# Kernel optimization log

Measured on AMD Instinct MI355X. Metric: run time of the kernel, lower is better.

The kernel has to match this reference:

```python
import jax, jax.numpy as jnp
import numpy as np
import math

B, L, C_IN, D, H, FACTOR = 32, 512, 32, 512, 8, 1
E = D // H
TOP_K = int(FACTOR * math.log(L))  # 6


def setup_inputs() -> dict:
    key = jax.random.key(0)
    ks = jax.random.split(key, 14)
    s = 0.02
    f = lambda k, shp: jax.random.normal(k, shp, jnp.float32) * s
    return {
        "x": jax.random.normal(ks[0], (B, L, C_IN), jnp.float32),
        "conv_w": f(ks[1], (D, C_IN)),  # Conv1d kernel_size=1 == pointwise linear
        "conv_b": f(ks[2], (D,)),
        "wq": f(ks[3], (D, D)), "bq": f(ks[4], (D,)),
        "wk": f(ks[5], (D, D)), "bk": f(ks[6], (D,)),
        "wv": f(ks[7], (D, D)), "bv": f(ks[8], (D,)),
        "wo": f(ks[9], (D, D)), "bo": f(ks[10], (D,)),
        "lin_w": f(ks[11], (1, D)), "lin_b": f(ks[12], (1,)),
    }


def _autocorrelation(q, k, v):
    # q, k, v: [B, L, H, E]; Autoformer AutoCorrelation (inference delay agg)
    qf = jnp.fft.rfft(q.transpose(0, 2, 3, 1), axis=-1)        # [B,H,E,Lf]
    kf = jnp.fft.rfft(k.transpose(0, 2, 3, 1), axis=-1)
    corr = jnp.fft.irfft(qf * jnp.conj(kf), n=L, axis=-1)       # [B,H,E,L]
    vals = v.transpose(0, 2, 3, 1)                              # [B,H,E,L]
    mean_corr = corr.mean(axis=(1, 2))                          # [B,L]
    weights, delay = jax.lax.top_k(mean_corr, TOP_K)            # [B,k]
    w = jax.nn.softmax(weights, axis=-1)                        # [B,k]
    # gather values at (t + delay) mod L  (== doubled-values trick in torch)
    idx = (jnp.arange(L)[None, None, :] + delay[:, :, None]) % L  # [B,k,L]
    patterns = jnp.take_along_axis(
        vals[:, :, :, None, :], idx[:, None, None, :, :], axis=-1)  # [B,H,E,k,L]
    agg = jnp.einsum('bhekl,bk->bhel', patterns, w)             # [B,H,E,L]
    return agg.transpose(0, 3, 1, 2)                            # [B,L,H,E]


def reference(x, conv_w, conv_b, wq, bq, wk, bk, wv, bv, wo, bo, lin_w, lin_b):
    # pointwise conv1d projection: [B,L,C_IN] -> [B,L,D]
    h = x @ conv_w.T + conv_b
    q = (h @ wq.T + bq).reshape(B, L, H, E)
    k = (h @ wk.T + bk).reshape(B, L, H, E)
    v = (h @ wv.T + bv).reshape(B, L, H, E)
    attn_out = _autocorrelation(q, k, v).reshape(B, L, D)
    new_x = attn_out @ wo.T + bo
    out = h + new_x          # residual
    last = out[:, -1:, :]    # x[:, -1:]
    y = last @ lin_w.T + lin_b  # [B,1,1]
    return y
```

## Files before the change

kernel.cpp:

```cpp
#include <hip/hip_runtime.h>
#include <hip/hip_bf16.h>

#define LL 512
#define BB 32
#define DD 512
#define CINN 32
#define TOPK 6
#define BL (BB * LL)

typedef __attribute__((ext_vector_type(8))) short bf16x8;
typedef __attribute__((ext_vector_type(4))) float f32x4;

__device__ inline float bf2f(ushort u) {
    union { uint i; float f; } c; c.i = ((uint)u) << 16; return c.f;
}
__device__ inline ushort f2bf(float f) {
    union { float f; uint i; } c; c.f = f;
    uint i = c.i;
    return (ushort)((i + 0x7FFFu + ((i >> 16) & 1u)) >> 16);
}
__device__ inline void split_bf(float v, ushort& hi, ushort& lo) {
    hi = f2bf(v);
    lo = f2bf(v - bf2f(hi));
}

__device__ inline void gload16(const ushort* g, ushort* l) {
    __builtin_amdgcn_global_load_lds(
        (const __attribute__((address_space(1))) unsigned int*)(const void*)g,
        (__attribute__((address_space(3))) unsigned int*)(void*)l,
        16, 0, 0);
}

__device__ inline void stage_tile32(ushort* buf,
                                    const ushort* A_h, const ushort* A_l,
                                    const ushort* B_h, const ushort* B_l,
                                    int wid, int lane) {
    const int l4 = lane >> 2, sl = lane & 3;
    const ushort* src = (wid == 0) ? A_h : (wid == 1) ? A_l : (wid == 2) ? B_h : B_l;
    ushort* dst = buf + wid * 4096;
    #pragma unroll
    for (int o = 0; o < 8; ++o) {
        const int row = o * 16 + l4;
        gload16(src + (long)row * 32 + ((sl ^ ((row >> 1) & 3)) << 3),
                dst + o * 512);
    }
}

__device__ inline bf16x8 frag_ld(const ushort* sm, int r, int s) {
    return *(const bf16x8*)(sm + r * 32 + ((s ^ ((r >> 1) & 3)) << 3));
}

__device__ inline void mfma_step(const ushort* sAh, const ushort* sAl,
                                 const ushort* sBh, const ushort* sBl,
                                 f32x4 acc[4][4], int wr, int wc, int fr, int fs) {
    bf16x8 bh[4], blo[4];
    #pragma unroll
    for (int ni = 0; ni < 4; ++ni) {
        bh[ni]  = frag_ld(sBh, wc + ni * 16 + fr, fs);
        blo[ni] = frag_ld(sBl, wc + ni * 16 + fr, fs);
    }
    #pragma unroll
    for (int mi = 0; mi < 4; ++mi) {
        const bf16x8 ah = frag_ld(sAh, wr + mi * 16 + fr, fs);
        const bf16x8 al = frag_ld(sAl, wr + mi * 16 + fr, fs);
        #pragma unroll
        for (int ni = 0; ni < 4; ++ni) {
            acc[mi][ni] = __builtin_amdgcn_mfma_f32_16x16x32_bf16(ah, bh[ni],  acc[mi][ni], 0, 0, 0);
            acc[mi][ni] = __builtin_amdgcn_mfma_f32_16x16x32_bf16(ah, blo[ni], acc[mi][ni], 0, 0, 0);
            acc[mi][ni] = __builtin_amdgcn_mfma_f32_16x16x32_bf16(al, bh[ni],  acc[mi][ni], 0, 0, 0);
        }
    }
}

__global__ __launch_bounds__(256) void prep_m(
    const float* __restrict__ wq, const float* __restrict__ wk,
    const float* __restrict__ cw,
    const float* __restrict__ lin_w, const float* __restrict__ wo,
    float* __restrict__ Mpart, float* __restrict__ upart)
{
    const int tid = threadIdx.x;
    if (blockIdx.x < 64) {
        __shared__ float cws[512][32];
        __shared__ float wqsT[512][9];
        __shared__ float wksT[512][9];
        __shared__ float aqs[8][32];
        __shared__ float aks[8][32];
        for (int i = tid; i < 4096; i += 256) {
            const int d = i >> 3, q = i & 7;
            *(float4*)&cws[d][q * 4] = *(const float4*)(cw + (long)d * 32 + q * 4);
        }
        const int e0 = blockIdx.x * 8;
        for (int i = tid; i < 4096; i += 256) {
            const int e = i >> 9, d = i & 511;
            wqsT[d][e] = wq[(long)(e0 + e) * 512 + d];
            wksT[d][e] = wk[(long)(e0 + e) * 512 + d];
        }
        __syncthreads();
        const int e_loc = tid >> 5, c = tid & 31;
        float aq = 0.f, ak = 0.f;
        #pragma unroll 4
        for (int d = 0; d < 512; ++d) {
            const float cv = cws[d][c];
            aq += wqsT[d][e_loc] * cv;
            ak += wksT[d][e_loc] * cv;
        }
        aqs[e_loc][c] = aq;
        aks[e_loc][c] = ak;
        __syncthreads();
        const int c_ = tid >> 3, cq = tid & 7;
        float m0 = 0.f, m1 = 0.f, m2 = 0.f, m3 = 0.f;
        #pragma unroll
        for (int e = 0; e < 8; ++e) {
            const float a = aqs[e][c_];
            const float4 k4 = *(const float4*)&aks[e][cq * 4];
            m0 += a * k4.x; m1 += a * k4.y; m2 += a * k4.z; m3 += a * k4.w;
        }
        *(float4*)(Mpart + (long)blockIdx.x * 1024 + c_ * 32 + cq * 4) =
            make_float4(m0, m1, m2, m3);
    } else {
        const int j = blockIdx.x - 64;
        const int n0 = j * 64;
        float u0 = 0.f, u1 = 0.f;
        for (int n = 0; n < 64; ++n) {
            const float lw = lin_w[n0 + n];
            u0 += lw * wo[(long)(n0 + n) * 512 + tid];
            u1 += lw * wo[(long)(n0 + n) * 512 + tid + 256];
        }
        upart[j * 512 + tid] = u0;
        upart[j * 512 + tid + 256] = u1;
    }
}

__global__ __launch_bounds__(256) void prep_xu(
    const float* __restrict__ x,
    const float* __restrict__ Mpart, const float* __restrict__ upart,
    const float* __restrict__ wv,
    ushort* __restrict__ Xh, ushort* __restrict__ Xl,
    ushort* __restrict__ Uh, ushort* __restrict__ Ul,
    float* __restrict__ v2part)
{
    const int tid = threadIdx.x;
    if (blockIdx.x < 64) {
        __shared__ float Ml[32][36];
        float s0 = 0.f, s1 = 0.f, s2 = 0.f, s3 = 0.f;
        for (int p = 0; p < 64; ++p) {
            const float4 v = *(const float4*)(Mpart + (long)p * 1024 + tid * 4);
            s0 += v.x; s1 += v.y; s2 += v.z; s3 += v.w;
        }
        const int mc_ = tid >> 3, mq = tid & 7;
        *(float4*)&Ml[mc_][mq * 4] = make_float4(s0, s1, s2, s3);
        __syncthreads();

        const long row = (long)blockIdx.x * 256 + tid;
        float xr[32], ur[32];
        #pragma unroll
        for (int q = 0; q < 8; ++q)
            *(float4*)&xr[q * 4] = *(const float4*)(x + row * 32 + q * 4);
        #pragma unroll
        for (int c2 = 0; c2 < 32; ++c2) {
            float s = 0.f;
            #pragma unroll
            for (int q = 0; q < 8; ++q) {
                const float4 m = *(const float4*)&Ml[c2][q * 4];
                s += m.x * xr[q * 4] + m.y * xr[q * 4 + 1]
                   + m.z * xr[q * 4 + 2] + m.w * xr[q * 4 + 3];
            }
            ur[c2] = s;
        }
        #pragma unroll
        for (int q = 0; q < 8; ++q) {
            ushort xh4[4], xl4[4], uh4[4], ul4[4];
            #pragma unroll
            for (int j = 0; j < 4; ++j) {
                split_bf(xr[q * 4 + j], xh4[j], xl4[j]);
                split_bf(ur[q * 4 + j], uh4[j], ul4[j]);
            }
            *(ushort4*)(Xh + row * 32 + q * 4) = make_ushort4(xh4[0], xh4[1], xh4[2], xh4[3]);
            *(ushort4*)(Xl + row * 32 + q * 4) = make_ushort4(xl4[0], xl4[1], xl4[2], xl4[3]);
            *(ushort4*)(Uh + row * 32 + q * 4) = make_ushort4(uh4[0], uh4[1], uh4[2], uh4[3]);
            *(ushort4*)(Ul + row * 32 + q * 4) = make_ushort4(ul4[0], ul4[1], ul4[2], ul4[3]);
        }
    } else {
        const int j = blockIdx.x - 64;
        __shared__ float us[64];
        if (tid < 64) {
            float s = 0.f;
            #pragma unroll
            for (int i = 0; i < 8; ++i) s += upart[i * 512 + j * 64 + tid];
            us[tid] = s;
        }
        __syncthreads();
        float s0 = 0.f, s1 = 0.f;
        for (int dl = 0; dl < 64; ++dl) {
            const float ud = us[dl];
            s0 += ud * wv[(long)(j * 64 + dl) * 512 + tid];
            s1 += ud * wv[(long)(j * 64 + dl) * 512 + tid + 256];
        }
        v2part[j * 512 + tid] = s0;
        v2part[j * 512 + tid + 256] = s1;
    }
}

__global__ __launch_bounds__(256) void corr_kernel(
    const ushort* __restrict__ Xh, const ushort* __restrict__ Xl,
    const ushort* __restrict__ Uh, const ushort* __restrict__ Ul,
    const float* __restrict__ v2part, const float* __restrict__ upart,
    const float* __restrict__ cw, const float* __restrict__ cb,
    const float* __restrict__ lin_w, const float* __restrict__ bv,
    const float* __restrict__ bo, const float* __restrict__ lin_b,
    float* __restrict__ mcpart, float* __restrict__ w34c)
{
    const int tid = threadIdx.x;
    if (blockIdx.x < 512) {
        __shared__ ushort buf[16384];
        __shared__ float mcloc[LL];
        const int wid = tid >> 6, lane = tid & 63;
        const int wr = (wid >> 1) * 64, wc = (wid & 1) * 64;
        const int fr = lane & 15, fs = lane >> 4;

        const int xcd = blockIdx.x & 7, s = blockIdx.x >> 3;
        const int b = xcd * 4 + (s >> 4);
        const int tile = s & 15;
        const int tm = tile >> 2, tn = tile & 3;

        const long abase = ((long)b * LL + tm * 128) * 32;
        const long bbase = ((long)b * LL + tn * 128) * 32;

        mcloc[tid] = 0.f; mcloc[tid + 256] = 0.f;

        stage_tile32(buf, Xh + abase, Xl + abase, Uh + bbase, Ul + bbase, wid, lane);
        __syncthreads();

        f32x4 acc[4][4] = {};
        mfma_step(buf, buf + 4096, buf + 8192, buf + 12288, acc, wr, wc, fr, fs);

        __syncthreads();
        const int base = wr - wc + 128 * (tm - tn) + fs * 4 - fr;
        #pragma unroll
        for (int k = -3; k <= 3; ++k) {
            #pragma unroll
            for (int r = 0; r < 4; ++r) {
                float sdg = 0.f;
                #pragma unroll
                for (int mi = 0; mi < 4; ++mi) {
                    const int ni = mi - k;
                    if (ni >= 0 && ni < 4) sdg += acc[mi][ni][r];
                }
                atomicAdd(&mcloc[(base + 16 * k + r) & (LL - 1)], sdg);
            }
        }
        __syncthreads();
        float* out = mcpart + ((long)b * 16 + tile) * LL;
        out[tid] = mcloc[tid];
        out[tid + 256] = mcloc[tid + 256];
    } else {
        __shared__ float v2s[512];
        __shared__ float us2[512];
        __shared__ float w3p[8][32];
        __shared__ float w4p[8][32];
        __shared__ float redc[4];
        {
            float a0 = 0.f, a1 = 0.f, b0 = 0.f, b1 = 0.f;
            #pragma unroll
            for (int i = 0; i < 8; ++i) {
                a0 += v2part[i * 512 + tid];
                a1 += v2part[i * 512 + tid + 256];
                b0 += upart[i * 512 + tid];
                b1 += upart[i * 512 + tid + 256];
            }
            v2s[tid] = a0; v2s[tid + 256] = a1;
            us2[tid] = b0; us2[tid + 256] = b1;
        }
        __syncthreads();
        const int c = tid & 31, g = tid >> 5;
        float w3 = 0.f, w4 = 0.f;
        for (int dl = 0; dl < 64; ++dl) {
            const int d = g * 64 + dl;
            const float cwv = cw[(long)d * 32 + c];
            w3 += v2s[d] * cwv;
            w4 += lin_w[d] * cwv;
        }
        w3p[g][c] = w3; w4p[g][c] = w4;
        __syncthreads();
        if (tid < 32) {
            float a3 = 0.f, a4 = 0.f;
            #pragma unroll
            for (int g2 = 0; g2 < 8; ++g2) { a3 += w3p[g2][tid]; a4 += w4p[g2][tid]; }
            w34c[tid] = a3;
            w34c[32 + tid] = a4;
        }
        float p = cb[tid] * (v2s[tid] + lin_w[tid])
                + cb[tid + 256] * (v2s[tid + 256] + lin_w[tid + 256])
                + bv[tid] * us2[tid] + bv[tid + 256] * us2[tid + 256]
                + bo[tid] * lin_w[tid] + bo[tid + 256] * lin_w[tid + 256];
        #pragma unroll
        for (int o = 32; o; o >>= 1) p += __shfl_down(p, o);
        if ((tid & 63) == 0) redc[tid >> 6] = p;
        __syncthreads();
        if (tid == 0) w34c[64] = redc[0] + redc[1] + redc[2] + redc[3] + lin_b[0];
    }
}

__global__ __launch_bounds__(256) void tail_kernel(
    const float* __restrict__ mcpart, const float* __restrict__ x,
    const float* __restrict__ w34c, float* __restrict__ out)
{
    const int b = blockIdx.x, tid = threadIdx.x;
    __shared__ float sv[256];
    __shared__ int   si[256];
    __shared__ float selv[TOPK];
    __shared__ int   seli[TOPK];
    __shared__ float wts[TOPK];

    float v0 = 0.f, v1 = 0.f;
    #pragma unroll
    for (int j = 0; j < 16; ++j) {
        v0 += mcpart[((long)b * 16 + j) * LL + tid];
        v1 += mcpart[((long)b * 16 + j) * LL + tid + 256];
    }
    v0 *= (1.0f / DD); v1 *= (1.0f / DD);

    int live0 = 1, live1 = 1;
    for (int r = 0; r < TOPK; ++r) {
        float bvv = -1e30f; int bi = -1;
        if (live0) { bvv = v0; bi = tid; }
        if (live1 && v1 > bvv) { bvv = v1; bi = tid + 256; }
        sv[tid] = bvv; si[tid] = bi;
        __syncthreads();
        for (int o = 128; o; o >>= 1) {
            if (tid < o) {
                const float ov = sv[tid + o]; const int oi = si[tid + o];
                if (ov > sv[tid] || (ov == sv[tid] && oi < si[tid])) { sv[tid] = ov; si[tid] = oi; }
            }
            __syncthreads();
        }
        if (tid == 0) { selv[r] = sv[0]; seli[r] = si[0]; }
        __syncthreads();
        const int w = seli[r];
        if (w == tid)       live0 = 0;
        if (w == tid + 256) live1 = 0;
        __syncthreads();
    }
    if (tid == 0) {
        const float mx = selv[0];
        float e[TOPK], ssum = 0.f;
        #pragma unroll
        for (int k = 0; k < TOPK; ++k) { e[k] = expf(selv[k] - mx); ssum += e[k]; }
        #pragma unroll
        for (int k = 0; k < TOPK; ++k) wts[k] = e[k] / ssum;
    }
    __syncthreads();

    if (tid < CINN) {
        float xm = 0.f;
        #pragma unroll
        for (int k = 0; k < TOPK; ++k) {
            const int r = (LL - 1 + seli[k]) & (LL - 1);
            xm += wts[k] * x[((long)b * LL + r) * CINN + tid];
        }
        const float xl = x[((long)b * LL + (LL - 1)) * CINN + tid];
        float yv = xl * w34c[32 + tid] + xm * w34c[tid];
        #pragma unroll
        for (int o = 16; o; o >>= 1) yv += __shfl_down(yv, o);
        if (tid == 0) out[b] = yv + w34c[64];
    }
}

extern "C" void kernel_launch(void* const* d_in, const int* in_sizes, int n_in,
                              void* d_out, int out_size, void* d_ws, size_t ws_size,
                              hipStream_t stream) {
    const float* x      = (const float*)d_in[0];
    const float* conv_w = (const float*)d_in[1];
    const float* conv_b = (const float*)d_in[2];
    const float* wq     = (const float*)d_in[3];
    const float* wk     = (const float*)d_in[5];
    const float* wv     = (const float*)d_in[7];
    const float* bv     = (const float*)d_in[8];
    const float* wo     = (const float*)d_in[9];
    const float* bo     = (const float*)d_in[10];
    const float* lin_w  = (const float*)d_in[11];
    const float* lin_b  = (const float*)d_in[12];

    char* w = (char*)d_ws;
    float* Mpart  = (float*)w;  w += (long)64 * 1024 * 4;
    float* upart  = (float*)w;  w += (long)8 * 512 * 4;
    float* v2part = (float*)w;  w += (long)8 * 512 * 4;
    float* w34c   = (float*)w;  w += 80 * 4;
    ushort* Xh    = (ushort*)w; w += (long)BL * 32 * 2;
    ushort* Xl    = (ushort*)w; w += (long)BL * 32 * 2;
    ushort* Uh    = (ushort*)w; w += (long)BL * 32 * 2;
    ushort* Ul    = (ushort*)w; w += (long)BL * 32 * 2;
    float* mcpart = (float*)w;  w += (long)BB * 16 * LL * 4;
    float* yout   = (float*)d_out;

    prep_m<<<72, 256, 0, stream>>>(wq, wk, conv_w, lin_w, wo, Mpart, upart);
    prep_xu<<<72, 256, 0, stream>>>(x, Mpart, upart, wv, Xh, Xl, Uh, Ul, v2part);
    corr_kernel<<<513, 256, 0, stream>>>(Xh, Xl, Uh, Ul, v2part, upart,
                                         conv_w, conv_b, lin_w, bv, bo, lin_b,
                                         mcpart, w34c);
    tail_kernel<<<BB, 256, 0, stream>>>(mcpart, x, w34c, yout);
}
```

Measured before the change: 65.48 us.

## Fuse bf16 split/U projection into correlation kernel and drop a launch

Merges the prep_xu stage into the correlation kernel. Each block now reduces Mpart, computes U = M·x for its tile and splits x and U into bf16 hi/lo pairs directly in LDS, so the Xh/Xl/Uh/Ul global round trip and one launch go away. The w34c scalar computation moves into the tail kernel, and the top-k reduction there uses wave shuffles instead of a shared-memory tree. In exchange every block recomputes the Mpart reduction and its U slice redundantly, and the tail kernel does more serial work per batch.

```diff
diff --git a/kernel.cpp b/kernel.cpp
--- a/kernel.cpp
+++ b/kernel.cpp
@@ -23,28 +23,7 @@
     hi = f2bf(v);
     lo = f2bf(v - bf2f(hi));
 }
-
-__device__ inline void gload16(const ushort* g, ushort* l) {
-    __builtin_amdgcn_global_load_lds(
-        (const __attribute__((address_space(1))) unsigned int*)(const void*)g,
-        (__attribute__((address_space(3))) unsigned int*)(void*)l,
-        16, 0, 0);
-}
-
-__device__ inline void stage_tile32(ushort* buf,
-                                    const ushort* A_h, const ushort* A_l,
-                                    const ushort* B_h, const ushort* B_l,
-                                    int wid, int lane) {
-    const int l4 = lane >> 2, sl = lane & 3;
-    const ushort* src = (wid == 0) ? A_h : (wid == 1) ? A_l : (wid == 2) ? B_h : B_l;
-    ushort* dst = buf + wid * 4096;
-    #pragma unroll
-    for (int o = 0; o < 8; ++o) {
-        const int row = o * 16 + l4;
-        gload16(src + (long)row * 32 + ((sl ^ ((row >> 1) & 3)) << 3),
-                dst + o * 512);
-    }
-}
+__device__ inline uint pk2(ushort a, ushort b) { return (uint)a | ((uint)b << 16); }
 
 __device__ inline bf16x8 frag_ld(const ushort* sm, int r, int s) {
     return *(const bf16x8*)(sm + r * 32 + ((s ^ ((r >> 1) & 3)) << 3));
@@ -131,57 +110,113 @@
     }
 }
 
-__global__ __launch_bounds__(256) void prep_xu(
+__global__ __launch_bounds__(256, 2) void corr_fused(
     const float* __restrict__ x,
     const float* __restrict__ Mpart, const float* __restrict__ upart,
     const float* __restrict__ wv,
-    ushort* __restrict__ Xh, ushort* __restrict__ Xl,
-    ushort* __restrict__ Uh, ushort* __restrict__ Ul,
-    float* __restrict__ v2part)
+    float* __restrict__ mcpart, float* __restrict__ v2part)
 {
     const int tid = threadIdx.x;
-    if (blockIdx.x < 64) {
+    if (blockIdx.x < 512) {
+        __shared__ ushort buf[16384];
         __shared__ float Ml[32][36];
-        float s0 = 0.f, s1 = 0.f, s2 = 0.f, s3 = 0.f;
-        for (int p = 0; p < 64; ++p) {
-            const float4 v = *(const float4*)(Mpart + (long)p * 1024 + tid * 4);
-            s0 += v.x; s1 += v.y; s2 += v.z; s3 += v.w;
-        }
-        const int mc_ = tid >> 3, mq = tid & 7;
-        *(float4*)&Ml[mc_][mq * 4] = make_float4(s0, s1, s2, s3);
-        __syncthreads();
-
-        const long row = (long)blockIdx.x * 256 + tid;
-        float xr[32], ur[32];
+        __shared__ float mcloc[LL];
+        ushort* bufAh = buf;
+        ushort* bufAl = buf + 4096;
+        ushort* bufBh = buf + 8192;
+        ushort* bufBl = buf + 12288;
+
+        const int xcd = blockIdx.x & 7, s = blockIdx.x >> 3;
+        const int b = xcd * 4 + (s >> 4);
+        const int tile = s & 15;
+        const int tm = tile >> 2, tn = tile & 3;
+
+        {
+            float4 ms = make_float4(0.f, 0.f, 0.f, 0.f);
+            for (int p = 0; p < 64; ++p) {
+                const float4 v = *(const float4*)(Mpart + (long)p * 1024 + tid * 4);
+                ms.x += v.x; ms.y += v.y; ms.z += v.z; ms.w += v.w;
+            }
+            *(float4*)&Ml[tid >> 3][(tid & 7) * 4] = ms;
+        }
+        mcloc[tid] = 0.f; mcloc[tid + 256] = 0.f;
+
+        const int r = tid >> 1;
+        const int pb = (tid & 1) * 2;
+        const int swz = (r >> 1) & 3;
+        const float* xA = x + ((long)b * LL + tm * 128 + r) * 32;
+        const float* xB = x + ((long)b * LL + tn * 128 + r) * 32;
+        float xb[32];
         #pragma unroll
         for (int q = 0; q < 8; ++q)
-            *(float4*)&xr[q * 4] = *(const float4*)(x + row * 32 + q * 4);
-        #pragma unroll
-        for (int c2 = 0; c2 < 32; ++c2) {
-            float s = 0.f;
-            #pragma unroll
-            for (int q = 0; q < 8; ++q) {
-                const float4 m = *(const float4*)&Ml[c2][q * 4];
-                s += m.x * xr[q * 4] + m.y * xr[q * 4 + 1]
-                   + m.z * xr[q * 4 + 2] + m.w * xr[q * 4 + 3];
+            *(float4*)&xb[q * 4] = *(const float4*)(xB + q * 4);
+
+        __syncthreads();
+
+        #pragma unroll
+        for (int pi = 0; pi < 2; ++pi) {
+            const int p = pb + pi;
+            const int sl = p ^ swz;
+            const int uoff = (r * 4 + p) * 8;
+            const float4 a0 = *(const float4*)(xA + sl * 8);
+            const float4 a1 = *(const float4*)(xA + sl * 8 + 4);
+            const float xe[8] = {a0.x, a0.y, a0.z, a0.w, a1.x, a1.y, a1.z, a1.w};
+            ushort xh[8], xl[8];
+            #pragma unroll
+            for (int j = 0; j < 8; ++j) split_bf(xe[j], xh[j], xl[j]);
+            *(uint4*)(bufAh + uoff) = make_uint4(pk2(xh[0], xh[1]), pk2(xh[2], xh[3]),
+                                                 pk2(xh[4], xh[5]), pk2(xh[6], xh[7]));
+            *(uint4*)(bufAl + uoff) = make_uint4(pk2(xl[0], xl[1]), pk2(xl[2], xl[3]),
+                                                 pk2(xl[4], xl[5]), pk2(xl[6], xl[7]));
+            float uv[8];
+            #pragma unroll
+            for (int j = 0; j < 8; ++j) {
+                const int c = sl * 8 + j;
+                float sacc = 0.f;
+                #pragma unroll
+                for (int q = 0; q < 8; ++q) {
+                    const float4 m = *(const float4*)&Ml[c][q * 4];
+                    sacc += m.x * xb[q * 4] + m.y * xb[q * 4 + 1]
+                          + m.z * xb[q * 4 + 2] + m.w * xb[q * 4 + 3];
+                }
+                uv[j] = sacc;
             }
-            ur[c2] = s;
-        }
-        #pragma unroll
-        for (int q = 0; q < 8; ++q) {
-            ushort xh4[4], xl4[4], uh4[4], ul4[4];
-            #pragma unroll
-            for (int j = 0; j < 4; ++j) {
-                split_bf(xr[q * 4 + j], xh4[j], xl4[j]);
-                split_bf(ur[q * 4 + j], uh4[j], ul4[j]);
+            ushort uh[8], ul[8];
+            #pragma unroll
+            for (int j = 0; j < 8; ++j) split_bf(uv[j], uh[j], ul[j]);
+            *(uint4*)(bufBh + uoff) = make_uint4(pk2(uh[0], uh[1]), pk2(uh[2], uh[3]),
+                                                 pk2(uh[4], uh[5]), pk2(uh[6], uh[7]));
+            *(uint4*)(bufBl + uoff) = make_uint4(pk2(ul[0], ul[1]), pk2(ul[2], ul[3]),
+                                                 pk2(ul[4], ul[5]), pk2(ul[6], ul[7]));
+        }
+        __syncthreads();
+
+        const int wid = tid >> 6, lane = tid & 63;
+        const int wr = (wid >> 1) * 64, wc = (wid & 1) * 64;
+        const int fr = lane & 15, fs = lane >> 4;
+        f32x4 acc[4][4] = {};
+        mfma_step(bufAh, bufAl, bufBh, bufBl, acc, wr, wc, fr, fs);
+
+        const int base = wr - wc + 128 * (tm - tn) + fs * 4 - fr;
+        #pragma unroll
+        for (int k = -3; k <= 3; ++k) {
+            #pragma unroll
+            for (int rr = 0; rr < 4; ++rr) {
+                float sdg = 0.f;
+                #pragma unroll
+                for (int mi = 0; mi < 4; ++mi) {
+                    const int ni = mi - k;
+                    if (ni >= 0 && ni < 4) sdg += acc[mi][ni][rr];
+                }
+                atomicAdd(&mcloc[(base + 16 * k + rr) & (LL - 1)], sdg);
             }
-            *(ushort4*)(Xh + row * 32 + q * 4) = make_ushort4(xh4[0], xh4[1], xh4[2], xh4[3]);
-            *(ushort4*)(Xl + row * 32 + q * 4) = make_ushort4(xl4[0], xl4[1], xl4[2], xl4[3]);
-            *(ushort4*)(Uh + row * 32 + q * 4) = make_ushort4(uh4[0], uh4[1], uh4[2], uh4[3]);
-            *(ushort4*)(Ul + row * 32 + q * 4) = make_ushort4(ul4[0], ul4[1], ul4[2], ul4[3]);
-        }
+        }
+        __syncthreads();
+        float* out = mcpart + ((long)b * 16 + tile) * LL;
+        out[tid] = mcloc[tid];
+        out[tid + 256] = mcloc[tid + 256];
     } else {
-        const int j = blockIdx.x - 64;
+        const int j = blockIdx.x - 512;
         __shared__ float us[64];
         if (tid < 64) {
             float s = 0.f;
@@ -201,77 +236,44 @@
     }
 }
 
-__global__ __launch_bounds__(256) void corr_kernel(
-    const ushort* __restrict__ Xh, const ushort* __restrict__ Xl,
-    const ushort* __restrict__ Uh, const ushort* __restrict__ Ul,
-    const float* __restrict__ v2part, const float* __restrict__ upart,
+__global__ __launch_bounds__(256) void tail_kernel(
+    const float* __restrict__ mcpart, const float* __restrict__ x,
+    const float* __restrict__ upart, const float* __restrict__ v2part,
     const float* __restrict__ cw, const float* __restrict__ cb,
     const float* __restrict__ lin_w, const float* __restrict__ bv,
     const float* __restrict__ bo, const float* __restrict__ lin_b,
-    float* __restrict__ mcpart, float* __restrict__ w34c)
+    float* __restrict__ out)
 {
-    const int tid = threadIdx.x;
-    if (blockIdx.x < 512) {
-        __shared__ ushort buf[16384];
-        __shared__ float mcloc[LL];
-        const int wid = tid >> 6, lane = tid & 63;
-        const int wr = (wid >> 1) * 64, wc = (wid & 1) * 64;
-        const int fr = lane & 15, fs = lane >> 4;
-
-        const int xcd = blockIdx.x & 7, s = blockIdx.x >> 3;
-        const int b = xcd * 4 + (s >> 4);
-        const int tile = s & 15;
-        const int tm = tile >> 2, tn = tile & 3;
-
-        const long abase = ((long)b * LL + tm * 128) * 32;
-        const long bbase = ((long)b * LL + tn * 128) * 32;
-
-        mcloc[tid] = 0.f; mcloc[tid + 256] = 0.f;
-
-        stage_tile32(buf, Xh + abase, Xl + abase, Uh + bbase, Ul + bbase, wid, lane);
-        __syncthreads();
-
-        f32x4 acc[4][4] = {};
-        mfma_step(buf, buf + 4096, buf + 8192, buf + 12288, acc, wr, wc, fr, fs);
-
-        __syncthreads();
-        const int base = wr - wc + 128 * (tm - tn) + fs * 4 - fr;
-        #pragma unroll
-        for (int k = -3; k <= 3; ++k) {
-            #pragma unroll
-            for (int r = 0; r < 4; ++r) {
-                float sdg = 0.f;
-                #pragma unroll
-                for (int mi = 0; mi < 4; ++mi) {
-                    const int ni = mi - k;
-                    if (ni >= 0 && ni < 4) sdg += acc[mi][ni][r];
-                }
-                atomicAdd(&mcloc[(base + 16 * k + r) & (LL - 1)], sdg);
-            }
-        }
-        __syncthreads();
-        float* out = mcpart + ((long)b * 16 + tile) * LL;
-        out[tid] = mcloc[tid];
-        out[tid + 256] = mcloc[tid + 256];
-    } else {
-        __shared__ float v2s[512];
-        __shared__ float us2[512];
-        __shared__ float w3p[8][32];
-        __shared__ float w4p[8][32];
-        __shared__ float redc[4];
-        {
-            float a0 = 0.f, a1 = 0.f, b0 = 0.f, b1 = 0.f;
-            #pragma unroll
-            for (int i = 0; i < 8; ++i) {
-                a0 += v2part[i * 512 + tid];
-                a1 += v2part[i * 512 + tid + 256];
-                b0 += upart[i * 512 + tid];
-                b1 += upart[i * 512 + tid + 256];
-            }
-            v2s[tid] = a0; v2s[tid + 256] = a1;
-            us2[tid] = b0; us2[tid + 256] = b1;
-        }
-        __syncthreads();
+    const int b = blockIdx.x, tid = threadIdx.x;
+    const int lane = tid & 63, wid = tid >> 6;
+    __shared__ float v2s[512];
+    __shared__ float us2[512];
+    __shared__ float w3p[8][32];
+    __shared__ float w4p[8][32];
+    __shared__ float w3s[32];
+    __shared__ float w4s[32];
+    __shared__ float c2s;
+    __shared__ float swv[4];
+    __shared__ int   swi[4];
+    __shared__ float selv[TOPK];
+    __shared__ int   seli[TOPK];
+    __shared__ float wts[TOPK];
+    __shared__ float redc[4];
+
+    {
+        float a0 = 0.f, a1 = 0.f, b0 = 0.f, b1 = 0.f;
+        #pragma unroll
+        for (int i = 0; i < 8; ++i) {
+            a0 += v2part[i * 512 + tid];
+            a1 += v2part[i * 512 + tid + 256];
+            b0 += upart[i * 512 + tid];
+            b1 += upart[i * 512 + tid + 256];
+        }
+        v2s[tid] = a0; v2s[tid + 256] = a1;
+        us2[tid] = b0; us2[tid + 256] = b1;
+    }
+    __syncthreads();
+    {
         const int c = tid & 31, g = tid >> 5;
         float w3 = 0.f, w4 = 0.f;
         for (int dl = 0; dl < 64; ++dl) {
@@ -281,14 +283,15 @@
             w4 += lin_w[d] * cwv;
         }
         w3p[g][c] = w3; w4p[g][c] = w4;
-        __syncthreads();
-        if (tid < 32) {
-            float a3 = 0.f, a4 = 0.f;
-            #pragma unroll
-            for (int g2 = 0; g2 < 8; ++g2) { a3 += w3p[g2][tid]; a4 += w4p[g2][tid]; }
-            w34c[tid] = a3;
-            w34c[32 + tid] = a4;
-        }
+    }
+    __syncthreads();
+    if (tid < 32) {
+        float a3 = 0.f, a4 = 0.f;
+        #pragma unroll
+        for (int g2 = 0; g2 < 8; ++g2) { a3 += w3p[g2][tid]; a4 += w4p[g2][tid]; }
+        w3s[tid] = a3; w4s[tid] = a4;
+    }
+    {
         float p = cb[tid] * (v2s[tid] + lin_w[tid])
                 + cb[tid + 256] * (v2s[tid + 256] + lin_w[tid + 256])
                 + bv[tid] * us2[tid] + bv[tid + 256] * us2[tid + 256]
@@ -296,21 +299,9 @@
         #pragma unroll
         for (int o = 32; o; o >>= 1) p += __shfl_down(p, o);
         if ((tid & 63) == 0) redc[tid >> 6] = p;
-        __syncthreads();
-        if (tid == 0) w34c[64] = redc[0] + redc[1] + redc[2] + redc[3] + lin_b[0];
-    }
-}
-
-__global__ __launch_bounds__(256) void tail_kernel(
-    const float* __restrict__ mcpart, const float* __restrict__ x,
-    const float* __restrict__ w34c, float* __restrict__ out)
-{
-    const int b = blockIdx.x, tid = threadIdx.x;
-    __shared__ float sv[256];
-    __shared__ int   si[256];
-    __shared__ float selv[TOPK];
-    __shared__ int   seli[TOPK];
-    __shared__ float wts[TOPK];
+    }
+    __syncthreads();
+    if (tid == 0) c2s = redc[0] + redc[1] + redc[2] + redc[3] + lin_b[0];
 
     float v0 = 0.f, v1 = 0.f;
     #pragma unroll
@@ -325,21 +316,26 @@
         float bvv = -1e30f; int bi = -1;
         if (live0) { bvv = v0; bi = tid; }
         if (live1 && v1 > bvv) { bvv = v1; bi = tid + 256; }
-        sv[tid] = bvv; si[tid] = bi;
-        __syncthreads();
-        for (int o = 128; o; o >>= 1) {
-            if (tid < o) {
-                const float ov = sv[tid + o]; const int oi = si[tid + o];
-                if (ov > sv[tid] || (ov == sv[tid] && oi < si[tid])) { sv[tid] = ov; si[tid] = oi; }
+        #pragma unroll
+        for (int o = 32; o; o >>= 1) {
+            const float ov = __shfl_down(bvv, o);
+            const int oi = __shfl_down(bi, o);
+            if (ov > bvv || (ov == bvv && oi < bi)) { bvv = ov; bi = oi; }
+        }
+        if (lane == 0) { swv[wid] = bvv; swi[wid] = bi; }
+        __syncthreads();
+        if (tid == 0) {
+            float fv = swv[0]; int fi = swi[0];
+            #pragma unroll
+            for (int w2 = 1; w2 < 4; ++w2) {
+                if (swv[w2] > fv || (swv[w2] == fv && swi[w2] < fi)) { fv = swv[w2]; fi = swi[w2]; }
             }
-            __syncthreads();
-        }
-        if (tid == 0) { selv[r] = sv[0]; seli[r] = si[0]; }
+            selv[r] = fv; seli[r] = fi;
+        }
         __syncthreads();
         const int w = seli[r];
         if (w == tid)       live0 = 0;
         if (w == tid + 256) live1 = 0;
-        __syncthreads();
     }
     if (tid == 0) {
         const float mx = selv[0];
@@ -358,11 +354,11 @@
             const int r = (LL - 1 + seli[k]) & (LL - 1);
             xm += wts[k] * x[((long)b * LL + r) * CINN + tid];
         }
-        const float xl = x[((long)b * LL + (LL - 1)) * CINN + tid];
-        float yv = xl * w34c[32 + tid] + xm * w34c[tid];
+        const float xlv = x[((long)b * LL + (LL - 1)) * CINN + tid];
+        float yv = xlv * w4s[tid] + xm * w3s[tid];
         #pragma unroll
         for (int o = 16; o; o >>= 1) yv += __shfl_down(yv, o);
-        if (tid == 0) out[b] = yv + w34c[64];
+        if (tid == 0) out[b] = yv + c2s;
     }
 }
 
@@ -385,18 +381,11 @@
     float* Mpart  = (float*)w;  w += (long)64 * 1024 * 4;
     float* upart  = (float*)w;  w += (long)8 * 512 * 4;
     float* v2part = (float*)w;  w += (long)8 * 512 * 4;
-    float* w34c   = (float*)w;  w += 80 * 4;
-    ushort* Xh    = (ushort*)w; w += (long)BL * 32 * 2;
-    ushort* Xl    = (ushort*)w; w += (long)BL * 32 * 2;
-    ushort* Uh    = (ushort*)w; w += (long)BL * 32 * 2;
-    ushort* Ul    = (ushort*)w; w += (long)BL * 32 * 2;
     float* mcpart = (float*)w;  w += (long)BB * 16 * LL * 4;
     float* yout   = (float*)d_out;
 
     prep_m<<<72, 256, 0, stream>>>(wq, wk, conv_w, lin_w, wo, Mpart, upart);
-    prep_xu<<<72, 256, 0, stream>>>(x, Mpart, upart, wv, Xh, Xl, Uh, Ul, v2part);
-    corr_kernel<<<513, 256, 0, stream>>>(Xh, Xl, Uh, Ul, v2part, upart,
-                                         conv_w, conv_b, lin_w, bv, bo, lin_b,
-                                         mcpart, w34c);
-    tail_kernel<<<BB, 256, 0, stream>>>(mcpart, x, w34c, yout);
-}
+    corr_fused<<<520, 256, 0, stream>>>(x, Mpart, upart, wv, mcpart, v2part);
+    tail_kernel<<<BB, 256, 0, stream>>>(mcpart, x, upart, v2part,
+                                        conv_w, conv_b, lin_w, bv, bo, lin_b, yout);
+}
```

New measurement: 61.75 us. 1.06x faster.
